# Optimization experiments

Measured on AMD Instinct MI355X. Metric: run time of the kernel, lower is better.

The kernel has to match this reference:

```python
import jax, jax.numpy as jnp
import numpy as np

B, C, H, W = 16, 256, 64, 64
E = 8           # num_experts
TOPK = 2
HID = int(C * 2.0)  # hidden_mult = 2.0 -> 512


def setup_inputs() -> dict:
    key = jax.random.key(0)
    ks = jax.random.split(key, 6)
    x = jax.random.normal(ks[0], (B, C, H, W), dtype=jnp.float32)
    Wr = jax.random.normal(ks[1], (C, E), dtype=jnp.float32) * 0.02
    br = jnp.zeros((E,), dtype=jnp.float32)
    W1 = jax.random.normal(ks[2], (E, C, HID), dtype=jnp.float32) * 0.02
    b1 = jnp.zeros((E, HID), dtype=jnp.float32)
    W2 = jax.random.normal(ks[3], (E, HID, C), dtype=jnp.float32) * 0.02
    b2 = jnp.zeros((E, C), dtype=jnp.float32)
    # nn.Parameter(torch.zeros(1)) in the original; use a small random value so
    scale = jax.random.normal(ks[4], (1,), dtype=jnp.float32) * 0.1
    return {"x": x, "Wr": Wr, "br": br, "W1": W1, "b1": b1,
            "W2": W2, "b2": b2, "scale": scale}


def reference(x, Wr, br, W1, b1, W2, b2, scale):
    b, c, h, w = x.shape
    tokens = jnp.transpose(x, (0, 2, 3, 1)).reshape(b, h * w, c)  # (B, T, C)
    logits = tokens @ Wr + br                                      # (B, T, E)
    topv, topi = jax.lax.top_k(logits, TOPK)                       # (B, T, K)
    wts = jax.nn.softmax(topv, axis=-1)                            # (B, T, K)

    out = jnp.zeros_like(tokens)
    num_experts = Wr.shape[1]
    for e in range(num_experts):
        # combine weight for expert e: sum of routing weights where selected
        we = jnp.sum(jnp.where(topi == e, wts, 0.0), axis=-1)      # (B, T)
        hdn = jax.nn.gelu(tokens @ W1[e] + b1[e], approximate=False)
        y = hdn @ W2[e] + b2[e]                                    # (B, T, C)
        out = out + y * we[..., None]

    out = jnp.transpose(out.reshape(b, h, w, c), (0, 3, 1, 2))     # (B, C, H, W)
    return x + scale[0] * out
```

## Files before the change

kernel.cpp:

```cpp
#include <hip/hip_runtime.h>
#include <hip/hip_bf16.h>
#include <math.h>

#define HW   4096
#define CCH  256
#define NE   8
#define HID  512
#define NTOK 65536
#define PADH 260

typedef short s16x8 __attribute__((ext_vector_type(8)));
typedef float f32x4 __attribute__((ext_vector_type(4)));

__global__ __launch_bounds__(256) void k_transpose_cast(
    const float* __restrict__ in, __hip_bfloat16* __restrict__ out, int R, int CC)
{
    __shared__ float t[64][65];
    int tilesC = CC >> 6;
    int per = (R >> 6) * tilesC;
    int e = blockIdx.x / per, tt = blockIdx.x % per;
    int r0 = (tt / tilesC) << 6, c0 = (tt % tilesC) << 6;
    const float* ip = in + (size_t)e * R * CC;
    __hip_bfloat16* op = out + (size_t)e * R * CC;
    int lane = threadIdx.x & 63, g = threadIdx.x >> 6;
    for (int i = 0; i < 16; i++) {
        int r = i * 4 + g;
        t[r][lane] = ip[(size_t)(r0 + r) * CC + c0 + lane];
    }
    __syncthreads();
    for (int i = 0; i < 16; i++) {
        int r = i * 4 + g;
        op[(size_t)(c0 + r) * R + r0 + lane] = __float2bfloat16(t[lane][r]);
    }
}

__global__ __launch_bounds__(256) void k_router(
    const float* __restrict__ x, const float* __restrict__ Wr, const float* __restrict__ br,
    __hip_bfloat16* __restrict__ tokens, int* __restrict__ pair, float2* __restrict__ wts,
    int* __restrict__ meta )
{
    __shared__ float xt[CCH][65];
    __shared__ float wr[CCH][NE];
    __shared__ float lg[64][NE];
    __shared__ int lc[NE];
    int tid = threadIdx.x;
    int n0 = blockIdx.x * 64;
    int b = n0 >> 12, p0 = n0 & 4095;
    const float* xb = x + (size_t)b * CCH * HW + p0;
    for (int i = tid; i < CCH * NE; i += 256) ((float*)wr)[i] = Wr[i];
    if (tid < NE) lc[tid] = 0;
    int lane = tid & 63, wv = tid >> 6;
    for (int i = 0; i < 64; i++) {
        int c = i * 4 + wv;
        xt[c][lane] = xb[(size_t)c * HW + lane];
    }
    __syncthreads();
    float a0 = br[2 * wv], a1 = br[2 * wv + 1];
    for (int c = 0; c < CCH; c++) {
        float xv = xt[c][lane];
        a0 = fmaf(xv, wr[c][2 * wv], a0);
        a1 = fmaf(xv, wr[c][2 * wv + 1], a1);
    }
    lg[lane][2 * wv] = a0;
    lg[lane][2 * wv + 1] = a1;
    __syncthreads();
    if (wv == 0) {
        float v0 = -1e30f, v1 = -1e30f; int i0 = 0, i1 = 0;
        for (int e = 0; e < NE; e++) {
            float l = lg[lane][e];
            if (l > v0)      { v1 = v0; i1 = i0; v0 = l; i0 = e; }
            else if (l > v1) { v1 = l; i1 = e; }
        }
        float e1 = expf(v1 - v0);
        float s = 1.0f + e1;
        wts[n0 + lane] = make_float2(1.0f / s, e1 / s);
        pair[n0 + lane] = i0 | (i1 << 8);
        atomicAdd(&lc[i0], 1);
        atomicAdd(&lc[i1], 1);
    }
    __syncthreads();
    if (tid < NE && lc[tid] > 0) atomicAdd(&meta[tid], lc[tid]);
    for (int r = 0; r < 64; r++)
        tokens[(size_t)(n0 + r) * CCH + tid] = __float2bfloat16(xt[tid][r]);
}

__global__ void k_scan(int* meta)
{
    if (threadIdx.x == 0) {
        int off = 0, toff = 0;
        for (int e = 0; e < NE; e++) {
            meta[16 + e] = off;
            meta[25 + e] = toff;
            int c = meta[e];
            off += c;
            toff += (c + 63) >> 6;
        }
        meta[24] = off;
        meta[33] = toff;
        meta[34] = toff;
    }
}

__global__ __launch_bounds__(256) void k_scatter(
    const int* __restrict__ pair, const float2* __restrict__ wts,
    int* __restrict__ meta, int* __restrict__ assign_tok, float* __restrict__ assign_w,
    int2* __restrict__ tok_slots)
{
    __shared__ int lcount[NE];
    __shared__ int lbase[NE];
    int tid = threadIdx.x;
    int n = blockIdx.x * 256 + tid;
    if (tid < NE) lcount[tid] = 0;
    __syncthreads();
    int pr = pair[n];
    int e0 = pr & 0xff, e1 = (pr >> 8) & 0xff;
    int p0 = atomicAdd(&lcount[e0], 1);
    int p1 = atomicAdd(&lcount[e1], 1);
    __syncthreads();
    if (tid < NE) lbase[tid] = atomicAdd(&meta[8 + tid], lcount[tid]);
    __syncthreads();
    float2 w = wts[n];
    int s0 = meta[16 + e0] + lbase[e0] + p0;
    int s1 = meta[16 + e1] + lbase[e1] + p1;
    assign_tok[s0] = n; assign_w[s0] = w.x;
    assign_tok[s1] = n; assign_w[s1] = w.y;
    tok_slots[n] = make_int2(s0, s1);
}

__global__ __launch_bounds__(512, 4) void k_expert(
    const __hip_bfloat16* __restrict__ tokens,
    const __hip_bfloat16* __restrict__ w1t,
    const __hip_bfloat16* __restrict__ w2t,
    const float* __restrict__ b1, const float* __restrict__ b2,
    const int* __restrict__ meta,
    const int* __restrict__ assign_tok, const float* __restrict__ assign_w,
    __hip_bfloat16* __restrict__ ybuf)
{
    __shared__ __align__(16) __hip_bfloat16 Af[64 * 256];
    __shared__ __align__(16) __hip_bfloat16 Hs[64 * PADH];
    __shared__ float wrow[64];
    __shared__ int trow[64];

    int total = meta[34];
    int bid = blockIdx.x;
    if (bid >= total) return;
    int e = 0;
    while (e < 7 && bid >= meta[25 + e + 1]) e++;
    int tile = bid - meta[25 + e];
    int cnt = meta[e];
    int r0 = tile << 6;
    int abase = meta[16 + e] + r0;
    int nrows = cnt - r0; if (nrows > 64) nrows = 64;

    int tid = threadIdx.x;
    if (tid < 64) {
        if (tid < nrows) { trow[tid] = assign_tok[abase + tid]; wrow[tid] = assign_w[abase + tid]; }
        else             { trow[tid] = 0; wrow[tid] = 0.0f; }
    }
    __syncthreads();

    {
        uint4* dst = (uint4*)Af;
#pragma unroll
        for (int j = 0; j < 4; j++) {
            int row = j * 16 + (tid & 15);
            int chunk = (tid >> 4) & 31;
            dst[j * 512 + tid] = ((const uint4*)(tokens + (size_t)trow[row] * CCH))[chunk];
        }
    }

    int lane = tid & 63, wv = tid >> 6;
    int quad = lane >> 4, l15 = lane & 15;

    const __hip_bfloat16* w1e = w1t + (size_t)e * HID * CCH;
    const __hip_bfloat16* w2e = w2t + (size_t)e * CCH * HID;
    const float* b1e = b1 + e * HID;

    const s16x8* apb = (const s16x8*)Af + quad * 16 + l15;

    f32x4 oacc[4][2];
#pragma unroll
    for (int i = 0; i < 4; i++)
#pragma unroll
        for (int j = 0; j < 2; j++) oacc[i][j] = (f32x4){0.f, 0.f, 0.f, 0.f};

    __syncthreads();

#pragma unroll
    for (int h = 0; h < 2; h++) {
        int c0 = h * 256 + wv * 32;
        const s16x8* bp0 = (const s16x8*)(w1e + (size_t)(c0)      * CCH + quad * 8);
        const s16x8* bp1 = (const s16x8*)(w1e + (size_t)(c0 + 16) * CCH + quad * 8);
        const s16x8* bq0 = (const s16x8*)((const __hip_bfloat16*)bp0 + (size_t)l15 * CCH);
        const s16x8* bq1 = (const s16x8*)((const __hip_bfloat16*)bp1 + (size_t)l15 * CCH);

        f32x4 hacc[4][2];
#pragma unroll
        for (int i = 0; i < 4; i++)
#pragma unroll
            for (int j = 0; j < 2; j++) hacc[i][j] = (f32x4){0.f, 0.f, 0.f, 0.f};

        s16x8 bf0 = bq0[0], bf1 = bq1[0];
#pragma unroll
        for (int kk = 0; kk < 8; kk++) {
            s16x8 bn0, bn1;
            if (kk < 7) { bn0 = bq0[(kk + 1) * 4]; bn1 = bq1[(kk + 1) * 4]; }
            s16x8 af[4];
#pragma unroll
            for (int mt = 0; mt < 4; mt++) af[mt] = apb[mt * 512 + kk * 4 * 16];
#pragma unroll
            for (int mt = 0; mt < 4; mt++) {
                hacc[mt][0] = __builtin_amdgcn_mfma_f32_16x16x32_bf16(af[mt], bf0, hacc[mt][0], 0, 0, 0);
                hacc[mt][1] = __builtin_amdgcn_mfma_f32_16x16x32_bf16(af[mt], bf1, hacc[mt][1], 0, 0, 0);
            }
            bf0 = bn0; bf1 = bn1;
        }

        __syncthreads();
#pragma unroll
        for (int nt = 0; nt < 2; nt++) {
            int cl = wv * 32 + nt * 16 + l15;
            float bias = b1e[h * 256 + cl];
#pragma unroll
            for (int mt = 0; mt < 4; mt++)
#pragma unroll
                for (int r = 0; r < 4; r++) {
                    int row = mt * 16 + quad * 4 + r;
                    float v = hacc[mt][nt][r] + bias;
                    float g = 0.5f * v * (1.0f + erff(v * 0.70710678118654752f));
                    Hs[row * PADH + cl] = __float2bfloat16(g);
                }
        }
        __syncthreads();

        const s16x8* b2q0 = (const s16x8*)(w2e + (size_t)(wv * 32      + l15) * HID + h * 256 + quad * 8);
        const s16x8* b2q1 = (const s16x8*)(w2e + (size_t)(wv * 32 + 16 + l15) * HID + h * 256 + quad * 8);

        s16x8 cf0 = b2q0[0], cf1 = b2q1[0];
#pragma unroll
        for (int kk = 0; kk < 8; kk++) {
            s16x8 cn0, cn1;
            if (kk < 7) { cn0 = b2q0[(kk + 1) * 4]; cn1 = b2q1[(kk + 1) * 4]; }
            s16x8 hf[4];
#pragma unroll
            for (int mt = 0; mt < 4; mt++)
                hf[mt] = *(const s16x8*)(Hs + (mt * 16 + l15) * PADH + kk * 32 + quad * 8);
#pragma unroll
            for (int mt = 0; mt < 4; mt++) {
                oacc[mt][0] = __builtin_amdgcn_mfma_f32_16x16x32_bf16(hf[mt], cf0, oacc[mt][0], 0, 0, 0);
                oacc[mt][1] = __builtin_amdgcn_mfma_f32_16x16x32_bf16(hf[mt], cf1, oacc[mt][1], 0, 0, 0);
            }
            cf0 = cn0; cf1 = cn1;
        }
        if (h == 0) __syncthreads();
    }

    const float* b2e = b2 + e * CCH;
#pragma unroll
    for (int nt = 0; nt < 2; nt++) {
        int cc = wv * 32 + nt * 16 + l15;
        float bias = b2e[cc];
#pragma unroll
        for (int mt = 0; mt < 4; mt++) {
#pragma unroll
            for (int r = 0; r < 4; r++) {
                int row = mt * 16 + quad * 4 + r;
                if (row < nrows) {
                    float v = (oacc[mt][nt][r] + bias) * wrow[row];
                    ybuf[(size_t)(abase + row) * CCH + cc] = __float2bfloat16(v);
                }
            }
        }
    }
}

__global__ __launch_bounds__(256) void k_combine(
    const float* __restrict__ x, const __hip_bfloat16* __restrict__ ybuf,
    const int2* __restrict__ tok_slots, const float* __restrict__ scale,
    float* __restrict__ out)
{
    __shared__ float moe[CCH][65];
    __shared__ int2 slots[64];
    int tid = threadIdx.x;
    int n0 = blockIdx.x * 64;
    if (tid < 64) slots[tid] = tok_slots[n0 + tid];
    __syncthreads();
    for (int r = 0; r < 64; r++) {
        int2 s = slots[r];
        float y = __bfloat162float(ybuf[(size_t)s.x * CCH + tid]) +
                  __bfloat162float(ybuf[(size_t)s.y * CCH + tid]);
        moe[tid][r] = y;
    }
    __syncthreads();
    float sc = scale[0];
    int b = n0 >> 12, p0 = n0 & 4095;
    const float* xb = x + (size_t)b * CCH * HW + p0;
    float* ob = out + (size_t)b * CCH * HW + p0;
    int lane = tid & 63, wv = tid >> 6;
    for (int i = 0; i < 64; i++) {
        int c = i * 4 + wv;
        ob[(size_t)c * HW + lane] = xb[(size_t)c * HW + lane] + sc * moe[c][lane];
    }
}

extern "C" void kernel_launch(void* const* d_in, const int* in_sizes, int n_in,
                              void* d_out, int out_size, void* d_ws, size_t ws_size,
                              hipStream_t stream)
{
    const float* x     = (const float*)d_in[0];
    const float* Wr    = (const float*)d_in[1];
    const float* br    = (const float*)d_in[2];
    const float* W1    = (const float*)d_in[3];
    const float* b1    = (const float*)d_in[4];
    const float* W2    = (const float*)d_in[5];
    const float* b2    = (const float*)d_in[6];
    const float* scale = (const float*)d_in[7];
    float* out = (float*)d_out;

    char* ws = (char*)d_ws;
    __hip_bfloat16* tokens = (__hip_bfloat16*)(ws);
    __hip_bfloat16* w1t    = (__hip_bfloat16*)(ws + 33554432);
    __hip_bfloat16* w2t    = (__hip_bfloat16*)(ws + 35651584);
    __hip_bfloat16* ybuf   = (__hip_bfloat16*)(ws + 37748736);
    int*    assign_tok = (int*)   (ws + 104857600);
    float*  assign_w   = (float*) (ws + 105381888);
    int2*   tok_slots  = (int2*)  (ws + 105906176);
    int*    pair       = (int*)   (ws + 106430464);
    float2* wts        = (float2*)(ws + 106692608);
    int*    meta       = (int*)   (ws + 107216896);

    hipMemsetAsync(meta, 0, 64, stream);
    k_transpose_cast<<<256, 256, 0, stream>>>(W1, w1t, 256, 512);
    k_transpose_cast<<<256, 256, 0, stream>>>(W2, w2t, 512, 256);
    k_router<<<1024, 256, 0, stream>>>(x, Wr, br, tokens, pair, wts, meta);
    k_scan<<<1, 64, 0, stream>>>(meta);
    k_scatter<<<256, 256, 0, stream>>>(pair, wts, meta, assign_tok, assign_w, tok_slots);
    k_expert<<<2056, 512, 0, stream>>>(tokens, w1t, w2t, b1, b2, meta,
                                       assign_tok, assign_w, ybuf);
    k_combine<<<1024, 256, 0, stream>>>(x, ybuf, tok_slots, scale, out);
}
```

Before: 369.6 us.

## Shrink expert tiles to 32 rows, fuse setup kernels, use fast GELU

The expert kernel moves from 64-row tiles with 512 threads to 32-row tiles with 256 threads. Each wave now computes 64 output columns, issues B-operand loads across passes, and raises its scheduling priority around the MFMA groups. The exact erf GELU becomes an exp2/rcp sigmoid approximation. The two weight transposes are merged into one launch, and the prefix-scan kernel is folded into the scatter kernel, which cuts launches. The aim is better occupancy and less launch overhead, at the cost of some GELU accuracy and more redundant weight reads per token.

Result: slower. 466.4 us (+26.2%).

```diff
diff --git a/kernel.cpp b/kernel.cpp
--- a/kernel.cpp
+++ b/kernel.cpp
@@ -12,13 +12,25 @@
 typedef short s16x8 __attribute__((ext_vector_type(8)));
 typedef float f32x4 __attribute__((ext_vector_type(4)));
 
-__global__ __launch_bounds__(256) void k_transpose_cast(
-    const float* __restrict__ in, __hip_bfloat16* __restrict__ out, int R, int CC)
+__device__ __forceinline__ float fast_gelu(float v) {
+    float v2 = v * v;
+    float s  = v * fmaf(0.10294324f, v2, 2.3022079f);
+    float e  = exp2f(-s);
+    return v * __builtin_amdgcn_rcpf(1.0f + e);
+}
+
+__global__ __launch_bounds__(256) void k_transpose_both(
+    const float* __restrict__ W1, const float* __restrict__ W2,
+    __hip_bfloat16* __restrict__ w1t, __hip_bfloat16* __restrict__ w2t)
 {
     __shared__ float t[64][65];
+    int bb = blockIdx.x;
+    const float* in; __hip_bfloat16* out; int R, CC;
+    if (bb < 256) { in = W1; out = w1t; R = 256; CC = 512; }
+    else          { in = W2; out = w2t; R = 512; CC = 256; bb -= 256; }
     int tilesC = CC >> 6;
     int per = (R >> 6) * tilesC;
-    int e = blockIdx.x / per, tt = blockIdx.x % per;
+    int e = bb / per, tt = bb % per;
     int r0 = (tt / tilesC) << 6, c0 = (tt % tilesC) << 6;
     const float* ip = in + (size_t)e * R * CC;
     __hip_bfloat16* op = out + (size_t)e * R * CC;
@@ -84,23 +96,6 @@
         tokens[(size_t)(n0 + r) * CCH + tid] = __float2bfloat16(xt[tid][r]);
 }
 
-__global__ void k_scan(int* meta)
-{
-    if (threadIdx.x == 0) {
-        int off = 0, toff = 0;
-        for (int e = 0; e < NE; e++) {
-            meta[16 + e] = off;
-            meta[25 + e] = toff;
-            int c = meta[e];
-            off += c;
-            toff += (c + 63) >> 6;
-        }
-        meta[24] = off;
-        meta[33] = toff;
-        meta[34] = toff;
-    }
-}
-
 __global__ __launch_bounds__(256) void k_scatter(
     const int* __restrict__ pair, const float2* __restrict__ wts,
     int* __restrict__ meta, int* __restrict__ assign_tok, float* __restrict__ assign_w,
@@ -108,6 +103,7 @@
 {
     __shared__ int lcount[NE];
     __shared__ int lbase[NE];
+    __shared__ int soff[NE];
     int tid = threadIdx.x;
     int n = blockIdx.x * 256 + tid;
     if (tid < NE) lcount[tid] = 0;
@@ -117,17 +113,28 @@
     int p0 = atomicAdd(&lcount[e0], 1);
     int p1 = atomicAdd(&lcount[e1], 1);
     __syncthreads();
+    if (tid == 0) {
+        int off = 0, toff = 0;
+        for (int ee = 0; ee < NE; ee++) {
+            soff[ee] = off;
+            int c = meta[ee];
+            if (blockIdx.x == 0) { meta[16 + ee] = off; meta[25 + ee] = toff; }
+            off += c;
+            toff += (c + 31) >> 5;
+        }
+        if (blockIdx.x == 0) { meta[24] = off; meta[33] = toff; meta[34] = toff; }
+    }
     if (tid < NE) lbase[tid] = atomicAdd(&meta[8 + tid], lcount[tid]);
     __syncthreads();
     float2 w = wts[n];
-    int s0 = meta[16 + e0] + lbase[e0] + p0;
-    int s1 = meta[16 + e1] + lbase[e1] + p1;
+    int s0 = soff[e0] + lbase[e0] + p0;
+    int s1 = soff[e1] + lbase[e1] + p1;
     assign_tok[s0] = n; assign_w[s0] = w.x;
     assign_tok[s1] = n; assign_w[s1] = w.y;
     tok_slots[n] = make_int2(s0, s1);
 }
 
-__global__ __launch_bounds__(512, 4) void k_expert(
+__global__ __launch_bounds__(256, 4) void k_expert(
     const __hip_bfloat16* __restrict__ tokens,
     const __hip_bfloat16* __restrict__ w1t,
     const __hip_bfloat16* __restrict__ w2t,
@@ -136,10 +143,10 @@
     const int* __restrict__ assign_tok, const float* __restrict__ assign_w,
     __hip_bfloat16* __restrict__ ybuf)
 {
-    __shared__ __align__(16) __hip_bfloat16 Af[64 * 256];
-    __shared__ __align__(16) __hip_bfloat16 Hs[64 * PADH];
-    __shared__ float wrow[64];
-    __shared__ int trow[64];
+    __shared__ __align__(16) __hip_bfloat16 Af[32 * 256];
+    __shared__ __align__(16) __hip_bfloat16 Hs[32 * PADH];
+    __shared__ float wrow[32];
+    __shared__ int trow[32];
 
     int total = meta[34];
     int bid = blockIdx.x;
@@ -148,24 +155,27 @@
     while (e < 7 && bid >= meta[25 + e + 1]) e++;
     int tile = bid - meta[25 + e];
     int cnt = meta[e];
-    int r0 = tile << 6;
+    int r0 = tile << 5;
     int abase = meta[16 + e] + r0;
-    int nrows = cnt - r0; if (nrows > 64) nrows = 64;
+    int nrows = cnt - r0; if (nrows > 32) nrows = 32;
 
     int tid = threadIdx.x;
-    if (tid < 64) {
+    if (tid < 32) {
         if (tid < nrows) { trow[tid] = assign_tok[abase + tid]; wrow[tid] = assign_w[abase + tid]; }
         else             { trow[tid] = 0; wrow[tid] = 0.0f; }
     }
-    __syncthreads();
 
     {
+        int rA = tid & 15, rB = 16 + (tid & 15);
+        int tA = (rA < nrows) ? assign_tok[abase + rA] : 0;
+        int tB = (rB < nrows) ? assign_tok[abase + rB] : 0;
         uint4* dst = (uint4*)Af;
 #pragma unroll
         for (int j = 0; j < 4; j++) {
-            int row = j * 16 + (tid & 15);
-            int chunk = (tid >> 4) & 31;
-            dst[j * 512 + tid] = ((const uint4*)(tokens + (size_t)trow[row] * CCH))[chunk];
+            int tr = (j & 1) ? tB : tA;
+            int chunk = (tid >> 4) + (j >> 1) * 16;
+            dst[(j & 1) * 512 + (j >> 1) * 256 + tid] =
+                ((const uint4*)(tokens + (size_t)tr * CCH))[chunk];
         }
     }
 
@@ -184,94 +194,107 @@
 #pragma unroll
         for (int j = 0; j < 2; j++) oacc[i][j] = (f32x4){0.f, 0.f, 0.f, 0.f};
 
+#define G1P(H, ROW) ((const s16x8*)(w1e + (size_t)((H) * 256 + wv * 64 + (ROW) + l15) * CCH) + quad)
+#define G2P(H, ROW) ((const s16x8*)(w2e + (size_t)(wv * 64 + (ROW) + l15) * HID + (H) * 256) + quad)
+#define LOADNEXT(P0, P1) { q0 = (P0); q1 = (P1); bf0 = q0[0]; bf1 = q1[0]; }
+
+#define PASS(A0EXPR, A1EXPR, ACC0, ACC1, TAIL)                                 \
+    {                                                                          \
+        _Pragma("unroll")                                                      \
+        for (int kk = 0; kk < 8; kk++) {                                       \
+            s16x8 bn0, bn1;                                                    \
+            if (kk < 7) { bn0 = q0[(kk + 1) * 4]; bn1 = q1[(kk + 1) * 4]; }    \
+            s16x8 a0 = (A0EXPR), a1 = (A1EXPR);                                \
+            __builtin_amdgcn_s_setprio(1);                                     \
+            ACC0[0] = __builtin_amdgcn_mfma_f32_16x16x32_bf16(a0, bf0, ACC0[0], 0, 0, 0); \
+            ACC1[0] = __builtin_amdgcn_mfma_f32_16x16x32_bf16(a0, bf1, ACC1[0], 0, 0, 0); \
+            ACC0[1] = __builtin_amdgcn_mfma_f32_16x16x32_bf16(a1, bf0, ACC0[1], 0, 0, 0); \
+            ACC1[1] = __builtin_amdgcn_mfma_f32_16x16x32_bf16(a1, bf1, ACC1[1], 0, 0, 0); \
+            __builtin_amdgcn_s_setprio(0);                                     \
+            if (kk < 7) { bf0 = bn0; bf1 = bn1; }                              \
+        }                                                                      \
+        TAIL                                                                   \
+    }
+
+#define A1_0 apb[kk * 64]
+#define A1_1 apb[512 + kk * 64]
+#define A2_0 (*(const s16x8*)(Hs + (size_t)l15 * PADH + kk * 32 + quad * 8))
+#define A2_1 (*(const s16x8*)(Hs + (size_t)(16 + l15) * PADH + kk * 32 + quad * 8))
+
+    const s16x8 *q0 = G1P(0, 0), *q1 = G1P(0, 16);
+    s16x8 bf0 = q0[0], bf1 = q1[0];
+
     __syncthreads();
 
 #pragma unroll
     for (int h = 0; h < 2; h++) {
-        int c0 = h * 256 + wv * 32;
-        const s16x8* bp0 = (const s16x8*)(w1e + (size_t)(c0)      * CCH + quad * 8);
-        const s16x8* bp1 = (const s16x8*)(w1e + (size_t)(c0 + 16) * CCH + quad * 8);
-        const s16x8* bq0 = (const s16x8*)((const __hip_bfloat16*)bp0 + (size_t)l15 * CCH);
-        const s16x8* bq1 = (const s16x8*)((const __hip_bfloat16*)bp1 + (size_t)l15 * CCH);
-
         f32x4 hacc[4][2];
 #pragma unroll
         for (int i = 0; i < 4; i++)
 #pragma unroll
             for (int j = 0; j < 2; j++) hacc[i][j] = (f32x4){0.f, 0.f, 0.f, 0.f};
 
-        s16x8 bf0 = bq0[0], bf1 = bq1[0];
-#pragma unroll
-        for (int kk = 0; kk < 8; kk++) {
-            s16x8 bn0, bn1;
-            if (kk < 7) { bn0 = bq0[(kk + 1) * 4]; bn1 = bq1[(kk + 1) * 4]; }
-            s16x8 af[4];
-#pragma unroll
-            for (int mt = 0; mt < 4; mt++) af[mt] = apb[mt * 512 + kk * 4 * 16];
-#pragma unroll
-            for (int mt = 0; mt < 4; mt++) {
-                hacc[mt][0] = __builtin_amdgcn_mfma_f32_16x16x32_bf16(af[mt], bf0, hacc[mt][0], 0, 0, 0);
-                hacc[mt][1] = __builtin_amdgcn_mfma_f32_16x16x32_bf16(af[mt], bf1, hacc[mt][1], 0, 0, 0);
-            }
-            bf0 = bn0; bf1 = bn1;
-        }
+        PASS(A1_0, A1_1, hacc[0], hacc[1], LOADNEXT(G1P(h, 32), G1P(h, 48)));
+        PASS(A1_0, A1_1, hacc[2], hacc[3], LOADNEXT(G2P(h, 0), G2P(h, 16)));
+
+        float bias0 = b1e[h * 256 + wv * 64 + l15];
+        float bias1 = b1e[h * 256 + wv * 64 + 16 + l15];
+        float bias2 = b1e[h * 256 + wv * 64 + 32 + l15];
+        float bias3 = b1e[h * 256 + wv * 64 + 48 + l15];
 
         __syncthreads();
 #pragma unroll
-        for (int nt = 0; nt < 2; nt++) {
-            int cl = wv * 32 + nt * 16 + l15;
-            float bias = b1e[h * 256 + cl];
-#pragma unroll
-            for (int mt = 0; mt < 4; mt++)
+        for (int nt = 0; nt < 4; nt++) {
+            float bias = (nt == 0) ? bias0 : (nt == 1) ? bias1 : (nt == 2) ? bias2 : bias3;
+            int cl = wv * 64 + nt * 16 + l15;
+#pragma unroll
+            for (int mt = 0; mt < 2; mt++)
 #pragma unroll
                 for (int r = 0; r < 4; r++) {
                     int row = mt * 16 + quad * 4 + r;
-                    float v = hacc[mt][nt][r] + bias;
-                    float g = 0.5f * v * (1.0f + erff(v * 0.70710678118654752f));
-                    Hs[row * PADH + cl] = __float2bfloat16(g);
+                    float v = hacc[nt][mt][r] + bias;
+                    Hs[row * PADH + cl] = __float2bfloat16(fast_gelu(v));
                 }
         }
         __syncthreads();
 
-        const s16x8* b2q0 = (const s16x8*)(w2e + (size_t)(wv * 32      + l15) * HID + h * 256 + quad * 8);
-        const s16x8* b2q1 = (const s16x8*)(w2e + (size_t)(wv * 32 + 16 + l15) * HID + h * 256 + quad * 8);
-
-        s16x8 cf0 = b2q0[0], cf1 = b2q1[0];
-#pragma unroll
-        for (int kk = 0; kk < 8; kk++) {
-            s16x8 cn0, cn1;
-            if (kk < 7) { cn0 = b2q0[(kk + 1) * 4]; cn1 = b2q1[(kk + 1) * 4]; }
-            s16x8 hf[4];
-#pragma unroll
-            for (int mt = 0; mt < 4; mt++)
-                hf[mt] = *(const s16x8*)(Hs + (mt * 16 + l15) * PADH + kk * 32 + quad * 8);
-#pragma unroll
-            for (int mt = 0; mt < 4; mt++) {
-                oacc[mt][0] = __builtin_amdgcn_mfma_f32_16x16x32_bf16(hf[mt], cf0, oacc[mt][0], 0, 0, 0);
-                oacc[mt][1] = __builtin_amdgcn_mfma_f32_16x16x32_bf16(hf[mt], cf1, oacc[mt][1], 0, 0, 0);
-            }
-            cf0 = cn0; cf1 = cn1;
-        }
-        if (h == 0) __syncthreads();
+        PASS(A2_0, A2_1, oacc[0], oacc[1], LOADNEXT(G2P(h, 32), G2P(h, 48)));
+        if (h == 0) {
+            PASS(A2_0, A2_1, oacc[2], oacc[3], LOADNEXT(G1P(1, 0), G1P(1, 16)));
+        } else {
+            PASS(A2_0, A2_1, oacc[2], oacc[3], );
+        }
     }
 
     const float* b2e = b2 + e * CCH;
-#pragma unroll
-    for (int nt = 0; nt < 2; nt++) {
-        int cc = wv * 32 + nt * 16 + l15;
-        float bias = b2e[cc];
-#pragma unroll
-        for (int mt = 0; mt < 4; mt++) {
+    float bb0 = b2e[wv * 64 + l15];
+    float bb1 = b2e[wv * 64 + 16 + l15];
+    float bb2 = b2e[wv * 64 + 32 + l15];
+    float bb3 = b2e[wv * 64 + 48 + l15];
+#pragma unroll
+    for (int nt = 0; nt < 4; nt++) {
+        float bias = (nt == 0) ? bb0 : (nt == 1) ? bb1 : (nt == 2) ? bb2 : bb3;
+        int cc = wv * 64 + nt * 16 + l15;
+#pragma unroll
+        for (int mt = 0; mt < 2; mt++) {
 #pragma unroll
             for (int r = 0; r < 4; r++) {
                 int row = mt * 16 + quad * 4 + r;
                 if (row < nrows) {
-                    float v = (oacc[mt][nt][r] + bias) * wrow[row];
+                    float v = (oacc[nt][mt][r] + bias) * wrow[row];
                     ybuf[(size_t)(abase + row) * CCH + cc] = __float2bfloat16(v);
                 }
             }
         }
     }
+#undef G1P
+#undef G2P
+#undef LOADNEXT
+#undef PASS
+#undef A1_0
+#undef A1_1
+#undef A2_0
+#undef A2_1
 }
 
 __global__ __launch_bounds__(256) void k_combine(
@@ -330,12 +353,10 @@
     int*    meta       = (int*)   (ws + 107216896);
 
     hipMemsetAsync(meta, 0, 64, stream);
-    k_transpose_cast<<<256, 256, 0, stream>>>(W1, w1t, 256, 512);
-    k_transpose_cast<<<256, 256, 0, stream>>>(W2, w2t, 512, 256);
+    k_transpose_both<<<512, 256, 0, stream>>>(W1, W2, w1t, w2t);
     k_router<<<1024, 256, 0, stream>>>(x, Wr, br, tokens, pair, wts, meta);
-    k_scan<<<1, 64, 0, stream>>>(meta);
     k_scatter<<<256, 256, 0, stream>>>(pair, wts, meta, assign_tok, assign_w, tok_slots);
-    k_expert<<<2056, 512, 0, stream>>>(tokens, w1t, w2t, b1, b2, meta,
+    k_expert<<<4104, 256, 0, stream>>>(tokens, w1t, w2t, b1, b2, meta,
                                        assign_tok, assign_w, ybuf);
     k_combine<<<1024, 256, 0, stream>>>(x, ybuf, tok_slots, scale, out);
 }
```
